# Performance work log

Measured on AMD Instinct MI355X. Metric: run time of the kernel, lower is better.

The kernel has to match this reference:

```python
import jax, jax.numpy as jnp
import numpy as np

B, T, N, F_DIM = 8, 32, 64, 6
D, H, C = 128, 4, 32          # hidden, spatial heads, head dim
L_SP, L_T, TH = 3, 3, 4       # spatial layers, temporal layers, temporal heads
THD = D // TH                 # temporal head dim
E = N * (N - 1)


def _ln(x, g, b, eps=1e-5):
    mu = x.mean(-1, keepdims=True)
    var = ((x - mu) ** 2).mean(-1, keepdims=True)
    return (x - mu) * jax.lax.rsqrt(var + eps) * g + b


def setup_inputs() -> dict:
    key = jax.random.key(0)
    ks = iter(jax.random.split(key, 64))
    r = lambda *s: jax.random.normal(next(ks), s, jnp.float32) * 0.05
    src_n, dst_n = np.nonzero(~np.eye(N, dtype=bool))
    inp = {
        'input_frames': jax.random.normal(next(ks), (B, T, N, F_DIM), jnp.float32),
        'edge_attr_seq': jax.random.uniform(next(ks), (B, T, E, 1), jnp.float32),
        'proj_W': r(F_DIM, D), 'proj_b': r(D),
        'sp_Wq': r(L_SP, D, D), 'sp_bq': r(L_SP, D),
        'sp_Wk': r(L_SP, D, D), 'sp_bk': r(L_SP, D),
        'sp_Wv': r(L_SP, D, D), 'sp_bv': r(L_SP, D),
        'sp_We': r(L_SP, 1, D), 'sp_be': r(L_SP, D),
        'sp_Ws': r(L_SP, D, D), 'sp_bs': r(L_SP, D),
        'sp_lng': jnp.ones((L_SP, D), jnp.float32), 'sp_lnb': jnp.zeros((L_SP, D), jnp.float32),
        'temporal_pos': r(1, 512, D),
        't_Wqkv': r(L_T, D, 3 * D), 't_bqkv': r(L_T, 3 * D),
        't_Wo': r(L_T, D, D), 't_bo': r(L_T, D),
        't_ln1g': jnp.ones((L_T, D), jnp.float32), 't_ln1b': jnp.zeros((L_T, D), jnp.float32),
        't_W1': r(L_T, D, 4 * D), 't_b1': r(L_T, 4 * D),
        't_W2': r(L_T, 4 * D, D), 't_b2': r(L_T, D),
        't_ln2g': jnp.ones((L_T, D), jnp.float32), 't_ln2b': jnp.zeros((L_T, D), jnp.float32),
        'head_W1': r(D, D), 'head_b1': r(D),
        'head_W2': r(D, F_DIM), 'head_b2': r(F_DIM),
        'edge_index': jnp.asarray(np.stack([src_n, dst_n]), jnp.int32),
    }
    return inp


def _forward(input_frames, edge_attr_seq, proj_W, proj_b, sp_Wq, sp_bq, sp_Wk, sp_bk,
             sp_Wv, sp_bv, sp_We, sp_be, sp_Ws, sp_bs, sp_lng, sp_lnb, temporal_pos,
             t_Wqkv, t_bqkv, t_Wo, t_bo, t_ln1g, t_ln1b, t_W1, t_b1, t_W2, t_b2,
             t_ln2g, t_ln2b, head_W1, head_b1, head_W2, head_b2, edge_index):
    BT = B * T
    Nt = BT * N                                       # total batched nodes
    offs = jnp.arange(BT, dtype=edge_index.dtype) * N
    src = (edge_index[0][None, :] + offs[:, None]).reshape(-1)   # (BT*E,)
    dst = (edge_index[1][None, :] + offs[:, None]).reshape(-1)
    ea = edge_attr_seq.reshape(BT * E, 1)
    h = input_frames.reshape(Nt, F_DIM) @ proj_W + proj_b        # (Nt, D)

    scale = 1.0 / jnp.sqrt(jnp.float32(C))
    for l in range(L_SP):
        q = (h @ sp_Wq[l] + sp_bq[l]).reshape(Nt, H, C)
        k = (h @ sp_Wk[l] + sp_bk[l]).reshape(Nt, H, C)
        v = (h @ sp_Wv[l] + sp_bv[l]).reshape(Nt, H, C)
        e = (ea @ sp_We[l] + sp_be[l]).reshape(-1, H, C)         # (Et, H, C)
        kj = k[src] + e
        alpha = (q[dst] * kj).sum(-1) * scale                    # (Et, H)
        amax = jax.ops.segment_max(alpha, dst, num_segments=Nt)
        ae = jnp.exp(alpha - amax[dst])
        asum = jax.ops.segment_sum(ae, dst, num_segments=Nt)
        w = ae / asum[dst]                                       # segment softmax
        msg = (v[src] + e) * w[..., None]
        agg = jax.ops.segment_sum(msg, dst, num_segments=Nt).reshape(Nt, D)
        out = agg + h @ sp_Ws[l] + sp_bs[l]                      # root/skip term
        h = _ln(h + out, sp_lng[l], sp_lnb[l])

    z = h.reshape(B, T, N, D).transpose(0, 2, 1, 3).reshape(B * N, T, D)
    z = z + temporal_pos[:, :T, :]

    causal = jnp.tril(jnp.ones((T, T), bool))
    tscale = 1.0 / jnp.sqrt(jnp.float32(THD))
    for l in range(L_T):
        qkv = z @ t_Wqkv[l] + t_bqkv[l]
        q, k, v = jnp.split(qkv, 3, axis=-1)
        q = q.reshape(B * N, T, TH, THD)
        k = k.reshape(B * N, T, TH, THD)
        v = v.reshape(B * N, T, TH, THD)
        s = jnp.einsum('bqhd,bkhd->bhqk', q, k) * tscale
        s = jnp.where(causal, s, -jnp.inf)
        a = jax.nn.softmax(s, axis=-1)
        o = jnp.einsum('bhqk,bkhd->bqhd', a, v).reshape(B * N, T, D)
        o = o @ t_Wo[l] + t_bo[l]
        z = _ln(z + o, t_ln1g[l], t_ln1b[l])
        f = jax.nn.gelu(z @ t_W1[l] + t_b1[l], approximate=False) @ t_W2[l] + t_b2[l]
        z = _ln(z + f, t_ln2g[l], t_ln2b[l])

    h_last = z[:, -1, :].reshape(B, N, D)
    pred = jax.nn.gelu(h_last @ head_W1 + head_b1, approximate=False) @ head_W2 + head_b2
    return pred                                                  # (B, N, F)


def reference(input_frames, edge_attr_seq, proj_W, proj_b, sp_Wq, sp_bq, sp_Wk, sp_bk,
              sp_Wv, sp_bv, sp_We, sp_be, sp_Ws, sp_bs, sp_lng, sp_lnb, temporal_pos,
              t_Wqkv, t_bqkv, t_Wo, t_bo, t_ln1g, t_ln1b, t_W1, t_b1, t_W2, t_b2,
              t_ln2g, t_ln2b, head_W1, head_b1, head_W2, head_b2, edge_index):
    return _forward(input_frames, edge_attr_seq, proj_W, proj_b, sp_Wq, sp_bq, sp_Wk,
                    sp_bk, sp_Wv, sp_bv, sp_We, sp_be, sp_Ws, sp_bs, sp_lng, sp_lnb,
                    temporal_pos, t_Wqkv, t_bqkv, t_Wo, t_bo, t_ln1g, t_ln1b, t_W1,
                    t_b1, t_W2, t_b2, t_ln2g, t_ln2b, head_W1, head_b1, head_W2,
                    head_b2, edge_index)
```

## Files before the change

kernel.cpp:

```cpp
#include <hip/hip_runtime.h>
#include <hip/hip_bf16.h>
#include <math.h>

typedef __hip_bfloat16 bf16;
typedef short short8 __attribute__((ext_vector_type(8)));
typedef float floatx4 __attribute__((ext_vector_type(4)));

#define B_    8
#define T_    32
#define N_    64
#define F_    6
#define D_    128
#define E_    4032
#define BT_   256
#define BN_   512

__device__ __forceinline__ float gelu_exact(float x) {
    return 0.5f * x * (1.0f + erff(x * 0.70710678118654752f));
}
__device__ __forceinline__ float bfbits2f(short s) {
    unsigned int u = ((unsigned int)(unsigned short)s) << 16;
    return __uint_as_float(u);
}
__device__ __forceinline__ void ld32lds(const bf16* p, float* o) {
    const short8* sp = (const short8*)p;
#pragma unroll
    for (int i = 0; i < 4; i++) {
        short8 s = sp[i];
#pragma unroll
        for (int j = 0; j < 8; j++) o[i * 8 + j] = bfbits2f(s[j]);
    }
}

struct RepackDesc { const float* W; bf16* out; int K, N, ntt, ntoff, L, start; };
struct RepackArgs { RepackDesc d[8]; int total; };

__global__ void k_repack(RepackArgs ra) {
    int gid = blockIdx.x * blockDim.x + threadIdx.x;
    if (gid >= ra.total) return;
    int fi = 0;
    while (fi < 7 && gid >= ra.d[fi + 1].start) fi++;
    RepackDesc dd = ra.d[fi];
    int r = gid - dd.start;
    int lane = r & 63; r >>= 6;
    int ntiles = dd.N >> 4;
    int nt = r % ntiles; r /= ntiles;
    int ktiles = dd.K >> 5;
    int kt = r % ktiles;
    int l = r / ktiles;
    int quad = lane >> 4, cc = lane & 15;
    const float* Wl = dd.W + (size_t)l * dd.K * dd.N;
    bf16* o = dd.out + ((((size_t)l * ktiles + kt) * dd.ntt + nt + dd.ntoff) * 64 + lane) * 8;
    int kb = kt * 32 + quad * 8;
    int n = nt * 16 + cc;
#pragma unroll
    for (int j = 0; j < 8; j++)
        o[j] = __float2bfloat16(Wl[(size_t)(kb + j) * dd.N + n]);
}

__global__ void k_packbias(const float* __restrict__ bq, const float* __restrict__ bk,
                           const float* __restrict__ bv, float* __restrict__ out) {
    int i = blockIdx.x * blockDim.x + threadIdx.x;
    if (i >= 3 * 384) return;
    int l = i / 384, c = i % 384;
    float v = (c < 128) ? bq[l * 128 + c]
            : (c < 256) ? bk[l * 128 + c - 128]
                        : bv[l * 128 + c - 256];
    out[i] = v;
}

__global__ __launch_bounds__(512, 2)
void k_spatial3(const float* __restrict__ inp, const float* __restrict__ projW,
                const float* __restrict__ projB,
                const short8* __restrict__ BpQKV, const short8* __restrict__ BpWS,
                const float* __restrict__ spb, const float* __restrict__ bs,
                const float* __restrict__ lng, const float* __restrict__ lnb,
                const float* __restrict__ ea, const float* __restrict__ Weg,
                const float* __restrict__ beg, const float* __restrict__ tpos,
                float* __restrict__ z32g) {
    __shared__ short smem[32768];
    bf16* hb = (bf16*)smem;
    bf16* qk = (bf16*)(smem + 8192);
    bf16* Ps = (bf16*)(smem + 8192);
    float* aggf = (float*)(smem + 8192);
    float* fsm = (float*)(smem + 8192);
    bf16* Vt = (bf16*)(smem + 24576);

    int bt = blockIdx.x;
    int tid = threadIdx.x;
    int lane = tid & 63, w = tid >> 6;
    int quad = lane >> 4, col = lane & 15;
    int w4 = w & 3, wh = w >> 2;
    const float scale = 0.17677669529663687f;

    for (int i = tid; i < 896; i += 512)
        fsm[i] = (i < 768) ? projW[i] : projB[i - 768];
    __syncthreads();
    float hreg[32];
    if (w < 4) {
#pragma unroll
        for (int r = 0; r < 4; r++) {
            int n = w * 16 + quad * 4 + r;
            const float* xr = inp + (size_t)(bt * 64 + n) * F_;
            float xin[6];
#pragma unroll
            for (int k2 = 0; k2 < 6; k2++) xin[k2] = xr[k2];
#pragma unroll
            for (int tt = 0; tt < 8; tt++) {
                int c = tt * 16 + col;
                float a = fsm[768 + c];
#pragma unroll
                for (int k2 = 0; k2 < 6; k2++) a = fmaf(xin[k2], fsm[k2 * 128 + c], a);
                hreg[tt * 4 + r] = a;
                hb[n * 128 + c] = __float2bfloat16(a);
            }
        }
    }
    __syncthreads();

    for (int l = 0; l < 3; l++) {
        {
            floatx4 acc[12];
#pragma unroll
            for (int tt = 0; tt < 12; tt++) acc[tt] = (floatx4){0.f, 0.f, 0.f, 0.f};
            const short8* bpl = BpQKV + (size_t)l * 6144;
            for (int kt = 0; kt < 4; kt++) {
                short8 a = *(const short8*)&hb[(w4 * 16 + col) * 128 + kt * 32 + quad * 8];
                const short8* bp = bpl + (size_t)(kt * 24 + wh * 12) * 64 + lane;
#pragma unroll
                for (int tt = 0; tt < 12; tt++)
                    acc[tt] = __builtin_amdgcn_mfma_f32_16x16x32_bf16(a, bp[tt * 64], acc[tt], 0, 0, 0);
            }
            const float* bias = spb + l * 384;
#pragma unroll
            for (int tt = 0; tt < 12; tt++) {
                int c = wh * 192 + tt * 16 + col;
                float bv = bias[c];
#pragma unroll
                for (int r = 0; r < 4; r++) {
                    int row = w4 * 16 + quad * 4 + r;
                    bf16 v = __float2bfloat16(acc[tt][r] + bv);
                    if (c < 256) qk[row * 256 + c] = v;
                    else         Vt[(c - 256) * 64 + row] = v;
                }
            }
        }
        __syncthreads();
        int h = w4, half = wh;
        int hoff = h * 32;
        const float* Wel = Weg + l * 128 + hoff;
        const float* bel = beg + l * 128 + hoff;
        float qWe;
        {
            int dst = half * 32 + (lane & 31);
            float qr[32];
            ld32lds(&qk[dst * 256 + hoff], qr);
            float s0 = 0.f;
#pragma unroll
            for (int c2 = 0; c2 < 32; c2++) s0 = fmaf(qr[c2], Wel[c2], s0);
            qWe = s0;
        }
        float s[2][4][4], ev[2][4][4];
        {
            short8 aA[2], bB[4];
#pragma unroll
            for (int mtl = 0; mtl < 2; mtl++)
                aA[mtl] = *(const short8*)&qk[((half * 2 + mtl) * 16 + col) * 256 + hoff + quad * 8];
#pragma unroll
            for (int nt = 0; nt < 4; nt++)
                bB[nt] = *(const short8*)&qk[(nt * 16 + col) * 256 + 128 + hoff + quad * 8];
#pragma unroll
            for (int mtl = 0; mtl < 2; mtl++)
#pragma unroll
                for (int nt = 0; nt < 4; nt++) {
                    floatx4 acc = (floatx4){0.f, 0.f, 0.f, 0.f};
                    acc = __builtin_amdgcn_mfma_f32_16x16x32_bf16(aA[mtl], bB[nt], acc, 0, 0, 0);
#pragma unroll
                    for (int r = 0; r < 4; r++) s[mtl][nt][r] = acc[r];
                }
        }
        const float* eag = ea + (size_t)bt * E_;
        float mx[2][4], ls[2][4], ae[2][4], inv[2][4];
#pragma unroll
        for (int mtl = 0; mtl < 2; mtl++)
#pragma unroll
            for (int r = 0; r < 4; r++) {
                int m = half * 32 + mtl * 16 + quad * 4 + r;
                float qWeR = __shfl(qWe, mtl * 16 + quad * 4 + r, 64);
                float rmax = -1e30f;
#pragma unroll
                for (int nt = 0; nt < 4; nt++) {
                    int n = nt * 16 + col;
                    bool diag = (m == n);
                    int eid = diag ? 0 : (n * 63 + m - (m > n ? 1 : 0));
                    float eav = diag ? 0.f : eag[eid];
                    ev[mtl][nt][r] = eav;
                    float al = diag ? -1e30f
                                    : scale * (s[mtl][nt][r] + eav * qWeR);
                    s[mtl][nt][r] = al;
                    rmax = fmaxf(rmax, al);
                }
#pragma unroll
                for (int mk2 = 1; mk2 <= 8; mk2 <<= 1)
                    rmax = fmaxf(rmax, __shfl_xor(rmax, mk2, 64));
                float lsum = 0.f, aesum = 0.f;
#pragma unroll
                for (int nt = 0; nt < 4; nt++) {
                    float p = __expf(s[mtl][nt][r] - rmax);
                    s[mtl][nt][r] = p;
                    lsum += p;
                    aesum = fmaf(p, ev[mtl][nt][r], aesum);
                }
#pragma unroll
                for (int mk2 = 1; mk2 <= 8; mk2 <<= 1) {
                    lsum += __shfl_xor(lsum, mk2, 64);
                    aesum += __shfl_xor(aesum, mk2, 64);
                }
                ls[mtl][r] = lsum;
                ae[mtl][r] = aesum;
                inv[mtl][r] = 1.0f / lsum;
            }
        __syncthreads();
#pragma unroll
        for (int mtl = 0; mtl < 2; mtl++)
#pragma unroll
            for (int nt = 0; nt < 4; nt++) {
                int n = nt * 16 + col;
#pragma unroll
                for (int r = 0; r < 4; r++) {
                    int m = half * 32 + mtl * 16 + quad * 4 + r;
                    Ps[h * 4096 + m * 64 + n] = __float2bfloat16(s[mtl][nt][r]);
                }
            }
        floatx4 oacc[2][2];
#pragma unroll
        for (int mtl = 0; mtl < 2; mtl++)
#pragma unroll
            for (int ntB = 0; ntB < 2; ntB++) oacc[mtl][ntB] = (floatx4){0.f, 0.f, 0.f, 0.f};
        for (int kt = 0; kt < 2; kt++) {
            short8 aP[2], bV[2];
#pragma unroll
            for (int mtl = 0; mtl < 2; mtl++)
                aP[mtl] = *(const short8*)&Ps[h * 4096 + (half * 32 + mtl * 16 + col) * 64 + kt * 32 + quad * 8];
#pragma unroll
            for (int ntB = 0; ntB < 2; ntB++)
                bV[ntB] = *(const short8*)&Vt[(hoff + ntB * 16 + col) * 64 + kt * 32 + quad * 8];
#pragma unroll
            for (int mtl = 0; mtl < 2; mtl++)
#pragma unroll
                for (int ntB = 0; ntB < 2; ntB++)
                    oacc[mtl][ntB] = __builtin_amdgcn_mfma_f32_16x16x32_bf16(aP[mtl], bV[ntB], oacc[mtl][ntB], 0, 0, 0);
        }
        __syncthreads();
#pragma unroll
        for (int mtl = 0; mtl < 2; mtl++)
#pragma unroll
            for (int ntB = 0; ntB < 2; ntB++) {
                int c = hoff + ntB * 16 + col;
                float Wc = Wel[ntB * 16 + col];
                float bc = bel[ntB * 16 + col];
#pragma unroll
                for (int r = 0; r < 4; r++) {
                    int m = half * 32 + mtl * 16 + quad * 4 + r;
                    aggf[m * 128 + c] = fmaf(fmaf(ae[mtl][r], Wc, oacc[mtl][ntB][r]),
                                             inv[mtl][r], bc);
                }
            }
        __syncthreads();
        if (w < 4) {
            floatx4 acc2[8];
#pragma unroll
            for (int tt = 0; tt < 8; tt++) acc2[tt] = (floatx4){0.f, 0.f, 0.f, 0.f};
            const short8* bpl = BpWS + (size_t)l * 2048;
            for (int kt = 0; kt < 4; kt++) {
                short8 a = *(const short8*)&hb[(w * 16 + col) * 128 + kt * 32 + quad * 8];
                const short8* bp = bpl + (size_t)(kt * 8) * 64 + lane;
#pragma unroll
                for (int tt = 0; tt < 8; tt++)
                    acc2[tt] = __builtin_amdgcn_mfma_f32_16x16x32_bf16(a, bp[tt * 64], acc2[tt], 0, 0, 0);
            }
            const float* bsl = bs + l * 128;
            float vv[32], rs[4] = {0.f, 0.f, 0.f, 0.f};
#pragma unroll
            for (int tt = 0; tt < 8; tt++) {
                int c = tt * 16 + col;
                float bv = bsl[c];
#pragma unroll
                for (int r = 0; r < 4; r++) {
                    int row = w * 16 + quad * 4 + r;
                    float v = acc2[tt][r] + bv + aggf[row * 128 + c] + hreg[tt * 4 + r];
                    vv[tt * 4 + r] = v;
                    rs[r] += v;
                }
            }
#pragma unroll
            for (int m = 1; m <= 8; m <<= 1)
#pragma unroll
                for (int r = 0; r < 4; r++) rs[r] += __shfl_xor(rs[r], m, 64);
            float mean[4], vs[4] = {0.f, 0.f, 0.f, 0.f};
#pragma unroll
            for (int r = 0; r < 4; r++) mean[r] = rs[r] * (1.0f / 128.0f);
#pragma unroll
            for (int i = 0; i < 32; i++) {
                float d = vv[i] - mean[i & 3];
                vv[i] = d;
                vs[i & 3] += d * d;
            }
#pragma unroll
            for (int m = 1; m <= 8; m <<= 1)
#pragma unroll
                for (int r = 0; r < 4; r++) vs[r] += __shfl_xor(vs[r], m, 64);
            float inv2[4];
#pragma unroll
            for (int r = 0; r < 4; r++) inv2[r] = rsqrtf(vs[r] * (1.0f / 128.0f) + 1e-5f);
            const float* gl = lng + l * 128;
            const float* bl = lnb + l * 128;
            if (l < 2) {
#pragma unroll
                for (int tt = 0; tt < 8; tt++) {
                    int c = tt * 16 + col;
                    float gc = gl[c], bc = bl[c];
#pragma unroll
                    for (int r = 0; r < 4; r++) {
                        float y = vv[tt * 4 + r] * inv2[r] * gc + bc;
                        int n = w * 16 + quad * 4 + r;
                        hreg[tt * 4 + r] = y;
                        hb[n * 128 + c] = __float2bfloat16(y);
                    }
                }
            } else {
                int b = bt >> 5, t_ = bt & 31;
#pragma unroll
                for (int tt = 0; tt < 8; tt++) {
                    int c = tt * 16 + col;
                    float gc = gl[c], bc = bl[c], pc = tpos[t_ * 128 + c];
#pragma unroll
                    for (int r = 0; r < 4; r++) {
                        float y = vv[tt * 4 + r] * inv2[r] * gc + bc;
                        int n = w * 16 + quad * 4 + r;
                        z32g[((size_t)(b * 64 + n) * 32 + t_) * 128 + c] = y + pc;
                    }
                }
            }
        }
        __syncthreads();
    }
}

__global__ __launch_bounds__(256, 2)
void k_temporal3(const float* __restrict__ z32g,
                 const short8* __restrict__ BpQKV, const short8* __restrict__ BpWO,
                 const short8* __restrict__ BpW1, const short8* __restrict__ BpW2,
                 const float* __restrict__ bqkv, const float* __restrict__ bo,
                 const float* __restrict__ ln1g, const float* __restrict__ ln1b,
                 const float* __restrict__ b1, const float* __restrict__ b2,
                 const float* __restrict__ ln2g, const float* __restrict__ ln2b,
                 float* __restrict__ zlast) {
    __shared__ short smem[27392];
    bf16* zb  = (bf16*)smem;
    bf16* qk  = (bf16*)(smem + 4352);
    bf16* Ps  = (bf16*)(smem + 12800);
    bf16* Vt  = (bf16*)(smem + 17920);
    bf16* o16 = (bf16*)(smem + 23040);
    bf16* f1  = (bf16*)(smem + 4352);

    int bn = blockIdx.x;
    int tid = threadIdx.x;
    int lane = tid & 63, w = tid >> 6;
    int quad = lane >> 4, col = lane & 15;
    int rsel = w & 1, csel = w >> 1;
    const float scale = 0.17677669529663687f;

    for (int i = tid; i < 4096; i += 256) {
        float v = z32g[(size_t)bn * 4096 + i];
        zb[(i >> 7) * 136 + (i & 127)] = __float2bfloat16(v);
    }
    float zreg[32];
    if (w < 2) {
#pragma unroll
        for (int tt = 0; tt < 8; tt++)
#pragma unroll
            for (int r = 0; r < 4; r++)
                zreg[tt * 4 + r] = z32g[(size_t)bn * 4096 +
                                        (w * 16 + quad * 4 + r) * 128 + tt * 16 + col];
    }
    __syncthreads();

    for (int l = 0; l < 3; l++) {
        {
            floatx4 acc[12];
#pragma unroll
            for (int tt = 0; tt < 12; tt++) acc[tt] = (floatx4){0.f, 0.f, 0.f, 0.f};
            const short8* bpl = BpQKV + (size_t)l * 6144;
            for (int kt = 0; kt < 4; kt++) {
                short8 a = *(const short8*)&zb[(rsel * 16 + col) * 136 + kt * 32 + quad * 8];
                const short8* bp = bpl + (size_t)(kt * 24 + csel * 12) * 64 + lane;
#pragma unroll
                for (int tt = 0; tt < 12; tt++)
                    acc[tt] = __builtin_amdgcn_mfma_f32_16x16x32_bf16(a, bp[tt * 64], acc[tt], 0, 0, 0);
            }
            const float* bias = bqkv + l * 384;
#pragma unroll
            for (int tt = 0; tt < 12; tt++) {
                int c = csel * 192 + tt * 16 + col;
                float bv = bias[c];
#pragma unroll
                for (int r = 0; r < 4; r++) {
                    int row = rsel * 16 + quad * 4 + r;
                    bf16 v = __float2bfloat16(acc[tt][r] + bv);
                    if (c < 256) qk[row * 264 + c] = v;
                    else         Vt[(c - 256) * 40 + row] = v;
                }
            }
        }
        __syncthreads();
        {
            int h = w, hoff = h * 32;
            float s[2][2][4];
            short8 aA[2], bB[2];
#pragma unroll
            for (int mt = 0; mt < 2; mt++)
                aA[mt] = *(const short8*)&qk[(mt * 16 + col) * 264 + hoff + quad * 8];
#pragma unroll
            for (int nt = 0; nt < 2; nt++)
                bB[nt] = *(const short8*)&qk[(nt * 16 + col) * 264 + 128 + hoff + quad * 8];
#pragma unroll
            for (int mt = 0; mt < 2; mt++)
#pragma unroll
                for (int nt = 0; nt < 2; nt++) {
                    floatx4 acc = (floatx4){0.f, 0.f, 0.f, 0.f};
                    acc = __builtin_amdgcn_mfma_f32_16x16x32_bf16(aA[mt], bB[nt], acc, 0, 0, 0);
#pragma unroll
                    for (int r = 0; r < 4; r++) s[mt][nt][r] = acc[r];
                }
            float inv[2][4];
#pragma unroll
            for (int mt = 0; mt < 2; mt++)
#pragma unroll
                for (int r = 0; r < 4; r++) {
                    int m = mt * 16 + quad * 4 + r;
                    float rmax = -1e30f;
#pragma unroll
                    for (int nt = 0; nt < 2; nt++) {
                        int n = nt * 16 + col;
                        float al = (n > m) ? -1e30f : s[mt][nt][r] * scale;
                        s[mt][nt][r] = al;
                        rmax = fmaxf(rmax, al);
                    }
#pragma unroll
                    for (int mk2 = 1; mk2 <= 8; mk2 <<= 1)
                        rmax = fmaxf(rmax, __shfl_xor(rmax, mk2, 64));
                    float lsum = 0.f;
#pragma unroll
                    for (int nt = 0; nt < 2; nt++) {
                        float p = __expf(s[mt][nt][r] - rmax);
                        s[mt][nt][r] = p;
                        lsum += p;
                    }
#pragma unroll
                    for (int mk2 = 1; mk2 <= 8; mk2 <<= 1)
                        lsum += __shfl_xor(lsum, mk2, 64);
                    inv[mt][r] = 1.0f / lsum;
                }
#pragma unroll
            for (int mt = 0; mt < 2; mt++)
#pragma unroll
                for (int nt = 0; nt < 2; nt++) {
                    int n = nt * 16 + col;
#pragma unroll
                    for (int r = 0; r < 4; r++)
                        Ps[h * 1280 + (mt * 16 + quad * 4 + r) * 40 + n] =
                            __float2bfloat16(s[mt][nt][r]);
                }
            floatx4 oacc[2][2];
#pragma unroll
            for (int mt = 0; mt < 2; mt++)
#pragma unroll
                for (int nt = 0; nt < 2; nt++) oacc[mt][nt] = (floatx4){0.f, 0.f, 0.f, 0.f};
            short8 aP[2], bV[2];
#pragma unroll
            for (int mt = 0; mt < 2; mt++)
                aP[mt] = *(const short8*)&Ps[h * 1280 + (mt * 16 + col) * 40 + quad * 8];
#pragma unroll
            for (int nt = 0; nt < 2; nt++)
                bV[nt] = *(const short8*)&Vt[(hoff + nt * 16 + col) * 40 + quad * 8];
#pragma unroll
            for (int mt = 0; mt < 2; mt++)
#pragma unroll
                for (int nt = 0; nt < 2; nt++)
                    oacc[mt][nt] = __builtin_amdgcn_mfma_f32_16x16x32_bf16(aP[mt], bV[nt], oacc[mt][nt], 0, 0, 0);
#pragma unroll
            for (int mt = 0; mt < 2; mt++)
#pragma unroll
                for (int nt = 0; nt < 2; nt++) {
                    int c = hoff + nt * 16 + col;
#pragma unroll
                    for (int r = 0; r < 4; r++)
                        o16[(mt * 16 + quad * 4 + r) * 136 + c] =
                            __float2bfloat16(oacc[mt][nt][r] * inv[mt][r]);
                }
        }
        __syncthreads();
        if (w < 2) {
            floatx4 acc2[8];
#pragma unroll
            for (int tt = 0; tt < 8; tt++) acc2[tt] = (floatx4){0.f, 0.f, 0.f, 0.f};
            const short8* bpl = BpWO + (size_t)l * 2048;
            for (int kt = 0; kt < 4; kt++) {
                short8 a = *(const short8*)&o16[(w * 16 + col) * 136 + kt * 32 + quad * 8];
                const short8* bp = bpl + (size_t)(kt * 8) * 64 + lane;
#pragma unroll
                for (int tt = 0; tt < 8; tt++)
                    acc2[tt] = __builtin_amdgcn_mfma_f32_16x16x32_bf16(a, bp[tt * 64], acc2[tt], 0, 0, 0);
            }
            const float* bol = bo + l * 128;
            float vv[32], rs[4] = {0.f, 0.f, 0.f, 0.f};
#pragma unroll
            for (int tt = 0; tt < 8; tt++) {
                int c = tt * 16 + col;
                float bv = bol[c];
#pragma unroll
                for (int r = 0; r < 4; r++) {
                    float v = acc2[tt][r] + bv + zreg[tt * 4 + r];
                    vv[tt * 4 + r] = v;
                    rs[r] += v;
                }
            }
#pragma unroll
            for (int m = 1; m <= 8; m <<= 1)
#pragma unroll
                for (int r = 0; r < 4; r++) rs[r] += __shfl_xor(rs[r], m, 64);
            float mean[4], vs[4] = {0.f, 0.f, 0.f, 0.f};
#pragma unroll
            for (int r = 0; r < 4; r++) mean[r] = rs[r] * (1.0f / 128.0f);
#pragma unroll
            for (int i = 0; i < 32; i++) {
                float d = vv[i] - mean[i & 3];
                vv[i] = d;
                vs[i & 3] += d * d;
            }
#pragma unroll
            for (int m = 1; m <= 8; m <<= 1)
#pragma unroll
                for (int r = 0; r < 4; r++) vs[r] += __shfl_xor(vs[r], m, 64);
            float inv2[4];
#pragma unroll
            for (int r = 0; r < 4; r++) inv2[r] = rsqrtf(vs[r] * (1.0f / 128.0f) + 1e-5f);
            const float* gl = ln1g + l * 128;
            const float* bl = ln1b + l * 128;
#pragma unroll
            for (int tt = 0; tt < 8; tt++) {
                int c = tt * 16 + col;
                float gc = gl[c], bc = bl[c];
#pragma unroll
                for (int r = 0; r < 4; r++) {
                    float y = vv[tt * 4 + r] * inv2[r] * gc + bc;
                    int row = w * 16 + quad * 4 + r;
                    zreg[tt * 4 + r] = y;
                    zb[row * 136 + c] = __float2bfloat16(y);
                }
            }
        }
        __syncthreads();
        {
            floatx4 acc3[16];
#pragma unroll
            for (int tt = 0; tt < 16; tt++) acc3[tt] = (floatx4){0.f, 0.f, 0.f, 0.f};
            const short8* bpl = BpW1 + (size_t)l * 8192;
            for (int kt = 0; kt < 4; kt++) {
                short8 a = *(const short8*)&zb[(rsel * 16 + col) * 136 + kt * 32 + quad * 8];
                const short8* bp = bpl + (size_t)(kt * 32 + csel * 16) * 64 + lane;
#pragma unroll
                for (int tt = 0; tt < 16; tt++)
                    acc3[tt] = __builtin_amdgcn_mfma_f32_16x16x32_bf16(a, bp[tt * 64], acc3[tt], 0, 0, 0);
            }
            const float* b1l = b1 + l * 512;
#pragma unroll
            for (int tt = 0; tt < 16; tt++) {
                int c = csel * 256 + tt * 16 + col;
                float bv = b1l[c];
#pragma unroll
                for (int r = 0; r < 4; r++) {
                    float v = gelu_exact(acc3[tt][r] + bv);
                    f1[(rsel * 16 + quad * 4 + r) * 520 + c] = __float2bfloat16(v);
                }
            }
        }
        __syncthreads();
        if (w < 2) {
            floatx4 acc4[8];
#pragma unroll
            for (int tt = 0; tt < 8; tt++) acc4[tt] = (floatx4){0.f, 0.f, 0.f, 0.f};
            const short8* bpl = BpW2 + (size_t)l * 8192;
            for (int kt = 0; kt < 16; kt++) {
                short8 a = *(const short8*)&f1[(w * 16 + col) * 520 + kt * 32 + quad * 8];
                const short8* bp = bpl + (size_t)(kt * 8) * 64 + lane;
#pragma unroll
                for (int tt = 0; tt < 8; tt++)
                    acc4[tt] = __builtin_amdgcn_mfma_f32_16x16x32_bf16(a, bp[tt * 64], acc4[tt], 0, 0, 0);
            }
            const float* b2l = b2 + l * 128;
            float vv[32], rs[4] = {0.f, 0.f, 0.f, 0.f};
#pragma unroll
            for (int tt = 0; tt < 8; tt++) {
                int c = tt * 16 + col;
                float bv = b2l[c];
#pragma unroll
                for (int r = 0; r < 4; r++) {
                    float v = acc4[tt][r] + bv + zreg[tt * 4 + r];
                    vv[tt * 4 + r] = v;
                    rs[r] += v;
                }
            }
#pragma unroll
            for (int m = 1; m <= 8; m <<= 1)
#pragma unroll
                for (int r = 0; r < 4; r++) rs[r] += __shfl_xor(rs[r], m, 64);
            float mean[4], vs[4] = {0.f, 0.f, 0.f, 0.f};
#pragma unroll
            for (int r = 0; r < 4; r++) mean[r] = rs[r] * (1.0f / 128.0f);
#pragma unroll
            for (int i = 0; i < 32; i++) {
                float d = vv[i] - mean[i & 3];
                vv[i] = d;
                vs[i & 3] += d * d;
            }
#pragma unroll
            for (int m = 1; m <= 8; m <<= 1)
#pragma unroll
                for (int r = 0; r < 4; r++) vs[r] += __shfl_xor(vs[r], m, 64);
            float inv2[4];
#pragma unroll
            for (int r = 0; r < 4; r++) inv2[r] = rsqrtf(vs[r] * (1.0f / 128.0f) + 1e-5f);
            const float* gl = ln2g + l * 128;
            const float* bl = ln2b + l * 128;
#pragma unroll
            for (int tt = 0; tt < 8; tt++) {
                int c = tt * 16 + col;
                float gc = gl[c], bc = bl[c];
#pragma unroll
                for (int r = 0; r < 4; r++) {
                    float y = vv[tt * 4 + r] * inv2[r] * gc + bc;
                    int row = w * 16 + quad * 4 + r;
                    zreg[tt * 4 + r] = y;
                    if (l < 2) zb[row * 136 + c] = __float2bfloat16(y);
                    else if (row == 31) zlast[(size_t)bn * 128 + c] = y;
                }
            }
        }
        __syncthreads();
    }
}

__global__ __launch_bounds__(128)
void k_head(const float* __restrict__ zlast, const float* __restrict__ W1,
            const float* __restrict__ b1, const float* __restrict__ W2,
            const float* __restrict__ b2, float* __restrict__ out) {
    int bn = blockIdx.x;
    int d = threadIdx.x;
    __shared__ float zl[128], h1[128];
    zl[d] = zlast[(size_t)bn * 128 + d];
    __syncthreads();
    float acc = b1[d];
    for (int k = 0; k < 128; k++) acc = fmaf(zl[k], W1[k * 128 + d], acc);
    h1[d] = gelu_exact(acc);
    __syncthreads();
    if (d < F_) {
        float o = b2[d];
        for (int k = 0; k < 128; k++) o = fmaf(h1[k], W2[k * F_ + d], o);
        out[bn * F_ + d] = o;
    }
}

extern "C" void kernel_launch(void* const* d_in, const int* in_sizes, int n_in,
                              void* d_out, int out_size, void* d_ws, size_t ws_size,
                              hipStream_t stream) {
    const float* input_frames = (const float*)d_in[0];
    const float* edge_attr    = (const float*)d_in[1];
    const float* proj_W  = (const float*)d_in[2];
    const float* proj_b  = (const float*)d_in[3];
    const float* sp_Wq   = (const float*)d_in[4];
    const float* sp_bq   = (const float*)d_in[5];
    const float* sp_Wk   = (const float*)d_in[6];
    const float* sp_bk   = (const float*)d_in[7];
    const float* sp_Wv   = (const float*)d_in[8];
    const float* sp_bv   = (const float*)d_in[9];
    const float* sp_We   = (const float*)d_in[10];
    const float* sp_be   = (const float*)d_in[11];
    const float* sp_Ws   = (const float*)d_in[12];
    const float* sp_bs   = (const float*)d_in[13];
    const float* sp_lng  = (const float*)d_in[14];
    const float* sp_lnb  = (const float*)d_in[15];
    const float* tpos    = (const float*)d_in[16];
    const float* t_Wqkv  = (const float*)d_in[17];
    const float* t_bqkv  = (const float*)d_in[18];
    const float* t_Wo    = (const float*)d_in[19];
    const float* t_bo    = (const float*)d_in[20];
    const float* t_ln1g  = (const float*)d_in[21];
    const float* t_ln1b  = (const float*)d_in[22];
    const float* t_W1    = (const float*)d_in[23];
    const float* t_b1    = (const float*)d_in[24];
    const float* t_W2    = (const float*)d_in[25];
    const float* t_b2    = (const float*)d_in[26];
    const float* t_ln2g  = (const float*)d_in[27];
    const float* t_ln2b  = (const float*)d_in[28];
    const float* head_W1 = (const float*)d_in[29];
    const float* head_b1 = (const float*)d_in[30];
    const float* head_W2 = (const float*)d_in[31];
    const float* head_b2 = (const float*)d_in[32];

    float* f     = (float*)d_ws;
    float* z32g  = f;
    float* zlast = f + (1u << 21);
    float* spb   = f + (1u << 21) + 65536;
    bf16* BpBase = (bf16*)(f + (1u << 21) + 65536 + 2048);
    bf16* BpSPQKV = BpBase;
    bf16* BpWS    = BpSPQKV + 147456;
    bf16* BpTQKV  = BpWS + 49152;
    bf16* BpWO    = BpTQKV + 147456;
    bf16* BpW1    = BpWO + 49152;
    bf16* BpW2    = BpW1 + 196608;

    RepackArgs ra;
    int s = 0;
    auto mk = [&](int i, const float* W, bf16* out, int K, int N, int ntt, int ntoff, int L) {
        ra.d[i] = {W, out, K, N, ntt, ntoff, L, s};
        s += L * (K >> 5) * (N >> 4) * 64;
    };
    mk(0, sp_Wq, BpSPQKV, 128, 128, 24, 0, 3);
    mk(1, sp_Wk, BpSPQKV, 128, 128, 24, 8, 3);
    mk(2, sp_Wv, BpSPQKV, 128, 128, 24, 16, 3);
    mk(3, sp_Ws, BpWS, 128, 128, 8, 0, 3);
    mk(4, t_Wqkv, BpTQKV, 128, 384, 24, 0, 3);
    mk(5, t_Wo, BpWO, 128, 128, 8, 0, 3);
    mk(6, t_W1, BpW1, 128, 512, 32, 0, 3);
    mk(7, t_W2, BpW2, 512, 128, 8, 0, 3);
    ra.total = s;
    k_repack<<<(s + 255) / 256, 256, 0, stream>>>(ra);
    k_packbias<<<(3 * 384 + 255) / 256, 256, 0, stream>>>(sp_bq, sp_bk, sp_bv, spb);

    k_spatial3<<<BT_, 512, 0, stream>>>(
        input_frames, proj_W, proj_b,
        (const short8*)BpSPQKV, (const short8*)BpWS,
        spb, sp_bs, sp_lng, sp_lnb, edge_attr, sp_We, sp_be, tpos, z32g);

    k_temporal3<<<BN_, 256, 0, stream>>>(
        z32g, (const short8*)BpTQKV, (const short8*)BpWO,
        (const short8*)BpW1, (const short8*)BpW2,
        t_bqkv, t_bo, t_ln1g, t_ln1b, t_b1, t_b2, t_ln2g, t_ln2b, zlast);

    k_head<<<BN_, 128, 0, stream>>>(zlast, head_W1, head_b1, head_W2, head_b2,
                                    (float*)d_out);
}
```

Measured before the change: 312.9 us.

## Pad LDS layouts, stage edge attrs, split-bf16 P·V, MFMA head kernel

Several changes at once. The spatial kernel pads its LDS rows to reduce bank conflicts and stages each block's edge attributes into LDS. It gives P its own buffer so one barrier can be removed, at the cost of dropping occupancy to one block per CU. Both attention kernels store P as hi/lo bf16 pairs and run two MFMAs per tile for accuracy, which doubles that work. The head kernel is rewritten to use MFMA over 64 rows per block with bf16 zlast input, replacing 512 tiny blocks of scalar FMA loops.

```diff
diff --git a/kernel.cpp b/kernel.cpp
--- a/kernel.cpp
+++ b/kernel.cpp
@@ -33,13 +33,13 @@
 }
 
 struct RepackDesc { const float* W; bf16* out; int K, N, ntt, ntoff, L, start; };
-struct RepackArgs { RepackDesc d[8]; int total; };
+struct RepackArgs { RepackDesc d[9]; int total; };
 
 __global__ void k_repack(RepackArgs ra) {
     int gid = blockIdx.x * blockDim.x + threadIdx.x;
     if (gid >= ra.total) return;
     int fi = 0;
-    while (fi < 7 && gid >= ra.d[fi + 1].start) fi++;
+    while (fi < 8 && gid >= ra.d[fi + 1].start) fi++;
     RepackDesc dd = ra.d[fi];
     int r = gid - dd.start;
     int lane = r & 63; r >>= 6;
@@ -69,7 +69,7 @@
     out[i] = v;
 }
 
-__global__ __launch_bounds__(512, 2)
+__global__ __launch_bounds__(512, 1)
 void k_spatial3(const float* __restrict__ inp, const float* __restrict__ projW,
                 const float* __restrict__ projB,
                 const short8* __restrict__ BpQKV, const short8* __restrict__ BpWS,
@@ -78,13 +78,14 @@
                 const float* __restrict__ ea, const float* __restrict__ Weg,
                 const float* __restrict__ beg, const float* __restrict__ tpos,
                 float* __restrict__ z32g) {
-    __shared__ short smem[32768];
+    __shared__ short smem[61312];
     bf16* hb = (bf16*)smem;
-    bf16* qk = (bf16*)(smem + 8192);
-    bf16* Ps = (bf16*)(smem + 8192);
-    float* aggf = (float*)(smem + 8192);
-    float* fsm = (float*)(smem + 8192);
-    bf16* Vt = (bf16*)(smem + 24576);
+    bf16* qk = (bf16*)(smem + 8704);
+    float* aggf = (float*)(smem + 8704);
+    float* fsm = (float*)(smem + 8704);
+    bf16* Vt = (bf16*)(smem + 25600);
+    bf16* Ps = (bf16*)(smem + 34816);
+    float* EAs = (float*)(smem + 53248);
 
     int bt = blockIdx.x;
     int tid = threadIdx.x;
@@ -95,6 +96,10 @@
 
     for (int i = tid; i < 896; i += 512)
         fsm[i] = (i < 768) ? projW[i] : projB[i - 768];
+    {
+        const float* eag = ea + (size_t)bt * E_;
+        for (int i = tid; i < E_; i += 512) EAs[i] = eag[i];
+    }
     __syncthreads();
     float hreg[32];
     if (w < 4) {
@@ -112,7 +117,7 @@
 #pragma unroll
                 for (int k2 = 0; k2 < 6; k2++) a = fmaf(xin[k2], fsm[k2 * 128 + c], a);
                 hreg[tt * 4 + r] = a;
-                hb[n * 128 + c] = __float2bfloat16(a);
+                hb[n * 136 + c] = __float2bfloat16(a);
             }
         }
     }
@@ -125,7 +130,7 @@
             for (int tt = 0; tt < 12; tt++) acc[tt] = (floatx4){0.f, 0.f, 0.f, 0.f};
             const short8* bpl = BpQKV + (size_t)l * 6144;
             for (int kt = 0; kt < 4; kt++) {
-                short8 a = *(const short8*)&hb[(w4 * 16 + col) * 128 + kt * 32 + quad * 8];
+                short8 a = *(const short8*)&hb[(w4 * 16 + col) * 136 + kt * 32 + quad * 8];
                 const short8* bp = bpl + (size_t)(kt * 24 + wh * 12) * 64 + lane;
 #pragma unroll
                 for (int tt = 0; tt < 12; tt++)
@@ -140,8 +145,8 @@
                 for (int r = 0; r < 4; r++) {
                     int row = w4 * 16 + quad * 4 + r;
                     bf16 v = __float2bfloat16(acc[tt][r] + bv);
-                    if (c < 256) qk[row * 256 + c] = v;
-                    else         Vt[(c - 256) * 64 + row] = v;
+                    if (c < 256) qk[row * 264 + c] = v;
+                    else         Vt[(c - 256) * 72 + row] = v;
                 }
             }
         }
@@ -154,21 +159,26 @@
         {
             int dst = half * 32 + (lane & 31);
             float qr[32];
-            ld32lds(&qk[dst * 256 + hoff], qr);
-            float s0 = 0.f;
-#pragma unroll
-            for (int c2 = 0; c2 < 32; c2++) s0 = fmaf(qr[c2], Wel[c2], s0);
-            qWe = s0;
+            ld32lds(&qk[dst * 264 + hoff], qr);
+            float s0 = 0.f, s1 = 0.f, s2 = 0.f, s3 = 0.f;
+#pragma unroll
+            for (int c2 = 0; c2 < 32; c2 += 4) {
+                s0 = fmaf(qr[c2], Wel[c2], s0);
+                s1 = fmaf(qr[c2 + 1], Wel[c2 + 1], s1);
+                s2 = fmaf(qr[c2 + 2], Wel[c2 + 2], s2);
+                s3 = fmaf(qr[c2 + 3], Wel[c2 + 3], s3);
+            }
+            qWe = (s0 + s1) + (s2 + s3);
         }
         float s[2][4][4], ev[2][4][4];
         {
             short8 aA[2], bB[4];
 #pragma unroll
             for (int mtl = 0; mtl < 2; mtl++)
-                aA[mtl] = *(const short8*)&qk[((half * 2 + mtl) * 16 + col) * 256 + hoff + quad * 8];
+                aA[mtl] = *(const short8*)&qk[((half * 2 + mtl) * 16 + col) * 264 + hoff + quad * 8];
 #pragma unroll
             for (int nt = 0; nt < 4; nt++)
-                bB[nt] = *(const short8*)&qk[(nt * 16 + col) * 256 + 128 + hoff + quad * 8];
+                bB[nt] = *(const short8*)&qk[(nt * 16 + col) * 264 + 128 + hoff + quad * 8];
 #pragma unroll
             for (int mtl = 0; mtl < 2; mtl++)
 #pragma unroll
@@ -179,8 +189,8 @@
                     for (int r = 0; r < 4; r++) s[mtl][nt][r] = acc[r];
                 }
         }
-        const float* eag = ea + (size_t)bt * E_;
-        float mx[2][4], ls[2][4], ae[2][4], inv[2][4];
+        __syncthreads();
+        float ls[2][4], ae[2][4], inv[2][4];
 #pragma unroll
         for (int mtl = 0; mtl < 2; mtl++)
 #pragma unroll
@@ -193,7 +203,7 @@
                     int n = nt * 16 + col;
                     bool diag = (m == n);
                     int eid = diag ? 0 : (n * 63 + m - (m > n ? 1 : 0));
-                    float eav = diag ? 0.f : eag[eid];
+                    float eav = diag ? 0.f : EAs[eid];
                     ev[mtl][nt][r] = eav;
                     float al = diag ? -1e30f
                                     : scale * (s[mtl][nt][r] + eav * qWeR);
@@ -220,38 +230,47 @@
                 ae[mtl][r] = aesum;
                 inv[mtl][r] = 1.0f / lsum;
             }
-        __syncthreads();
+        bf16* PsH = Ps + h * 4608;
+        floatx4 oacc[2][2];
 #pragma unroll
         for (int mtl = 0; mtl < 2; mtl++)
 #pragma unroll
-            for (int nt = 0; nt < 4; nt++) {
-                int n = nt * 16 + col;
-#pragma unroll
-                for (int r = 0; r < 4; r++) {
-                    int m = half * 32 + mtl * 16 + quad * 4 + r;
-                    Ps[h * 4096 + m * 64 + n] = __float2bfloat16(s[mtl][nt][r]);
-                }
-            }
-        floatx4 oacc[2][2];
-#pragma unroll
-        for (int mtl = 0; mtl < 2; mtl++)
-#pragma unroll
             for (int ntB = 0; ntB < 2; ntB++) oacc[mtl][ntB] = (floatx4){0.f, 0.f, 0.f, 0.f};
-        for (int kt = 0; kt < 2; kt++) {
-            short8 aP[2], bV[2];
+#pragma unroll
+        for (int p = 0; p < 2; p++) {
 #pragma unroll
             for (int mtl = 0; mtl < 2; mtl++)
-                aP[mtl] = *(const short8*)&Ps[h * 4096 + (half * 32 + mtl * 16 + col) * 64 + kt * 32 + quad * 8];
+#pragma unroll
+                for (int q2 = 0; q2 < 2; q2++) {
+                    int nl = q2 * 16 + col;
+                    int base0 = (half * 32 + mtl * 16 + quad * 4) * 72 + ((nl >> 3) * 2) * 8 + (nl & 7);
+#pragma unroll
+                    for (int r = 0; r < 4; r++) {
+                        float p_ = s[mtl][2 * p + q2][r];
+                        bf16 hi = __float2bfloat16(p_);
+                        bf16 lo = __float2bfloat16(p_ - bfbits2f(*(short*)&hi));
+                        PsH[base0 + r * 72] = hi;
+                        PsH[base0 + r * 72 + 8] = lo;
+                    }
+                }
+            short8 aPh[2], aPl[2], bV[2];
+#pragma unroll
+            for (int mtl = 0; mtl < 2; mtl++) {
+                int rb = (half * 32 + mtl * 16 + col) * 72 + quad * 16;
+                aPh[mtl] = *(const short8*)&PsH[rb];
+                aPl[mtl] = *(const short8*)&PsH[rb + 8];
+            }
 #pragma unroll
             for (int ntB = 0; ntB < 2; ntB++)
-                bV[ntB] = *(const short8*)&Vt[(hoff + ntB * 16 + col) * 64 + kt * 32 + quad * 8];
+                bV[ntB] = *(const short8*)&Vt[(hoff + ntB * 16 + col) * 72 + p * 32 + quad * 8];
 #pragma unroll
             for (int mtl = 0; mtl < 2; mtl++)
 #pragma unroll
-                for (int ntB = 0; ntB < 2; ntB++)
-                    oacc[mtl][ntB] = __builtin_amdgcn_mfma_f32_16x16x32_bf16(aP[mtl], bV[ntB], oacc[mtl][ntB], 0, 0, 0);
-        }
-        __syncthreads();
+                for (int ntB = 0; ntB < 2; ntB++) {
+                    oacc[mtl][ntB] = __builtin_amdgcn_mfma_f32_16x16x32_bf16(aPh[mtl], bV[ntB], oacc[mtl][ntB], 0, 0, 0);
+                    oacc[mtl][ntB] = __builtin_amdgcn_mfma_f32_16x16x32_bf16(aPl[mtl], bV[ntB], oacc[mtl][ntB], 0, 0, 0);
+                }
+        }
 #pragma unroll
         for (int mtl = 0; mtl < 2; mtl++)
 #pragma unroll
@@ -273,7 +292,7 @@
             for (int tt = 0; tt < 8; tt++) acc2[tt] = (floatx4){0.f, 0.f, 0.f, 0.f};
             const short8* bpl = BpWS + (size_t)l * 2048;
             for (int kt = 0; kt < 4; kt++) {
-                short8 a = *(const short8*)&hb[(w * 16 + col) * 128 + kt * 32 + quad * 8];
+                short8 a = *(const short8*)&hb[(w * 16 + col) * 136 + kt * 32 + quad * 8];
                 const short8* bp = bpl + (size_t)(kt * 8) * 64 + lane;
 #pragma unroll
                 for (int tt = 0; tt < 8; tt++)
@@ -325,7 +344,7 @@
                         float y = vv[tt * 4 + r] * inv2[r] * gc + bc;
                         int n = w * 16 + quad * 4 + r;
                         hreg[tt * 4 + r] = y;
-                        hb[n * 128 + c] = __float2bfloat16(y);
+                        hb[n * 136 + c] = __float2bfloat16(y);
                     }
                 }
             } else {
@@ -355,13 +374,13 @@
                  const float* __restrict__ ln1g, const float* __restrict__ ln1b,
                  const float* __restrict__ b1, const float* __restrict__ b2,
                  const float* __restrict__ ln2g, const float* __restrict__ ln2b,
-                 float* __restrict__ zlast) {
-    __shared__ short smem[27392];
+                 bf16* __restrict__ zlastb) {
+    __shared__ short smem[31488];
     bf16* zb  = (bf16*)smem;
     bf16* qk  = (bf16*)(smem + 4352);
     bf16* Ps  = (bf16*)(smem + 12800);
-    bf16* Vt  = (bf16*)(smem + 17920);
-    bf16* o16 = (bf16*)(smem + 23040);
+    bf16* Vt  = (bf16*)(smem + 22016);
+    bf16* o16 = (bf16*)(smem + 27136);
     bf16* f1  = (bf16*)(smem + 4352);
 
     int bn = blockIdx.x;
@@ -416,6 +435,7 @@
         __syncthreads();
         {
             int h = w, hoff = h * 32;
+            bf16* PsH = Ps + h * 2304;
             float s[2][2][4];
             short8 aA[2], bB[2];
 #pragma unroll
@@ -467,28 +487,38 @@
 #pragma unroll
                 for (int nt = 0; nt < 2; nt++) {
                     int n = nt * 16 + col;
-#pragma unroll
-                    for (int r = 0; r < 4; r++)
-                        Ps[h * 1280 + (mt * 16 + quad * 4 + r) * 40 + n] =
-                            __float2bfloat16(s[mt][nt][r]);
+                    int base0 = (mt * 16 + quad * 4) * 72 + ((n >> 3) * 2) * 8 + (n & 7);
+#pragma unroll
+                    for (int r = 0; r < 4; r++) {
+                        float p_ = s[mt][nt][r];
+                        bf16 hi = __float2bfloat16(p_);
+                        bf16 lo = __float2bfloat16(p_ - bfbits2f(*(short*)&hi));
+                        PsH[base0 + r * 72] = hi;
+                        PsH[base0 + r * 72 + 8] = lo;
+                    }
                 }
             floatx4 oacc[2][2];
 #pragma unroll
             for (int mt = 0; mt < 2; mt++)
 #pragma unroll
                 for (int nt = 0; nt < 2; nt++) oacc[mt][nt] = (floatx4){0.f, 0.f, 0.f, 0.f};
-            short8 aP[2], bV[2];
-#pragma unroll
-            for (int mt = 0; mt < 2; mt++)
-                aP[mt] = *(const short8*)&Ps[h * 1280 + (mt * 16 + col) * 40 + quad * 8];
+            short8 aPh[2], aPl[2], bV[2];
+#pragma unroll
+            for (int mt = 0; mt < 2; mt++) {
+                int rb = (mt * 16 + col) * 72 + quad * 16;
+                aPh[mt] = *(const short8*)&PsH[rb];
+                aPl[mt] = *(const short8*)&PsH[rb + 8];
+            }
 #pragma unroll
             for (int nt = 0; nt < 2; nt++)
                 bV[nt] = *(const short8*)&Vt[(hoff + nt * 16 + col) * 40 + quad * 8];
 #pragma unroll
             for (int mt = 0; mt < 2; mt++)
 #pragma unroll
-                for (int nt = 0; nt < 2; nt++)
-                    oacc[mt][nt] = __builtin_amdgcn_mfma_f32_16x16x32_bf16(aP[mt], bV[nt], oacc[mt][nt], 0, 0, 0);
+                for (int nt = 0; nt < 2; nt++) {
+                    oacc[mt][nt] = __builtin_amdgcn_mfma_f32_16x16x32_bf16(aPh[mt], bV[nt], oacc[mt][nt], 0, 0, 0);
+                    oacc[mt][nt] = __builtin_amdgcn_mfma_f32_16x16x32_bf16(aPl[mt], bV[nt], oacc[mt][nt], 0, 0, 0);
+                }
 #pragma unroll
             for (int mt = 0; mt < 2; mt++)
 #pragma unroll
@@ -644,7 +674,7 @@
                     int row = w * 16 + quad * 4 + r;
                     zreg[tt * 4 + r] = y;
                     if (l < 2) zb[row * 136 + c] = __float2bfloat16(y);
-                    else if (row == 31) zlast[(size_t)bn * 128 + c] = y;
+                    else if (row == 31) zlastb[(size_t)bn * 128 + c] = __float2bfloat16(y);
                 }
             }
         }
@@ -652,23 +682,51 @@
     }
 }
 
-__global__ __launch_bounds__(128)
-void k_head(const float* __restrict__ zlast, const float* __restrict__ W1,
+__global__ __launch_bounds__(256)
+void k_head(const bf16* __restrict__ zlastb, const short8* __restrict__ BpHW1,
             const float* __restrict__ b1, const float* __restrict__ W2,
             const float* __restrict__ b2, float* __restrict__ out) {
-    int bn = blockIdx.x;
-    int d = threadIdx.x;
-    __shared__ float zl[128], h1[128];
-    zl[d] = zlast[(size_t)bn * 128 + d];
+    __shared__ bf16 h1[64 * 136];
+    int blk = blockIdx.x;
+    int tid = threadIdx.x;
+    int lane = tid & 63, w = tid >> 6;
+    int quad = lane >> 4, col = lane & 15;
+    {
+        floatx4 acc[8];
+#pragma unroll
+        for (int tt = 0; tt < 8; tt++) acc[tt] = (floatx4){0.f, 0.f, 0.f, 0.f};
+        const short8* Ap = (const short8*)(zlastb + (size_t)(blk * 64 + w * 16 + col) * 128) + quad;
+        for (int kt = 0; kt < 4; kt++) {
+            short8 a = Ap[kt * 4];
+            const short8* bp = BpHW1 + (size_t)(kt * 8) * 64 + lane;
+#pragma unroll
+            for (int tt = 0; tt < 8; tt++)
+                acc[tt] = __builtin_amdgcn_mfma_f32_16x16x32_bf16(a, bp[tt * 64], acc[tt], 0, 0, 0);
+        }
+#pragma unroll
+        for (int tt = 0; tt < 8; tt++) {
+            int c = tt * 16 + col;
+            float bv = b1[c];
+#pragma unroll
+            for (int r = 0; r < 4; r++)
+                h1[(w * 16 + quad * 4 + r) * 136 + c] = __float2bfloat16(gelu_exact(acc[tt][r] + bv));
+        }
+    }
     __syncthreads();
-    float acc = b1[d];
-    for (int k = 0; k < 128; k++) acc = fmaf(zl[k], W1[k * 128 + d], acc);
-    h1[d] = gelu_exact(acc);
-    __syncthreads();
-    if (d < F_) {
-        float o = b2[d];
-        for (int k = 0; k < 128; k++) o = fmaf(h1[k], W2[k * F_ + d], o);
-        out[bn * F_ + d] = o;
+    for (int idx = tid; idx < 512; idx += 256) {
+        int row = idx >> 3, c = idx & 7;
+        if (c < 6) {
+            float a0 = 0.f, a1 = 0.f, a2 = 0.f, a3 = 0.f;
+            const bf16* hr = &h1[row * 136];
+#pragma unroll 8
+            for (int k = 0; k < 128; k += 4) {
+                a0 = fmaf(bfbits2f(*(const short*)&hr[k]),     W2[k * 6 + c], a0);
+                a1 = fmaf(bfbits2f(*(const short*)&hr[k + 1]), W2[(k + 1) * 6 + c], a1);
+                a2 = fmaf(bfbits2f(*(const short*)&hr[k + 2]), W2[(k + 2) * 6 + c], a2);
+                a3 = fmaf(bfbits2f(*(const short*)&hr[k + 3]), W2[(k + 3) * 6 + c], a3);
+            }
+            out[(size_t)(blk * 64 + row) * 6 + c] = (a0 + a1) + (a2 + a3) + b2[c];
+        }
     }
 }
 
@@ -711,7 +769,7 @@
 
     float* f     = (float*)d_ws;
     float* z32g  = f;
-    float* zlast = f + (1u << 21);
+    bf16*  zlastb = (bf16*)(f + (1u << 21));
     float* spb   = f + (1u << 21) + 65536;
     bf16* BpBase = (bf16*)(f + (1u << 21) + 65536 + 2048);
     bf16* BpSPQKV = BpBase;
@@ -720,6 +778,7 @@
     bf16* BpWO    = BpTQKV + 147456;
     bf16* BpW1    = BpWO + 49152;
     bf16* BpW2    = BpW1 + 196608;
+    bf16* BpHW1   = BpW2 + 196608;
 
     RepackArgs ra;
     int s = 0;
@@ -735,6 +794,7 @@
     mk(5, t_Wo, BpWO, 128, 128, 8, 0, 3);
     mk(6, t_W1, BpW1, 128, 512, 32, 0, 3);
     mk(7, t_W2, BpW2, 512, 128, 8, 0, 3);
+    mk(8, head_W1, BpHW1, 128, 128, 8, 0, 1);
     ra.total = s;
     k_repack<<<(s + 255) / 256, 256, 0, stream>>>(ra);
     k_packbias<<<(3 * 384 + 255) / 256, 256, 0, stream>>>(sp_bq, sp_bk, sp_bv, spb);
@@ -747,8 +807,8 @@
     k_temporal3<<<BN_, 256, 0, stream>>>(
         z32g, (const short8*)BpTQKV, (const short8*)BpWO,
         (const short8*)BpW1, (const short8*)BpW2,
-        t_bqkv, t_bo, t_ln1g, t_ln1b, t_b1, t_b2, t_ln2g, t_ln2b, zlast);
-
-    k_head<<<BN_, 128, 0, stream>>>(zlast, head_W1, head_b1, head_W2, head_b2,
-                                    (float*)d_out);
+        t_bqkv, t_bo, t_ln1g, t_ln1b, t_b1, t_b2, t_ln2g, t_ln2b, zlastb);
+
+    k_head<<<8, 256, 0, stream>>>(zlastb, (const short8*)BpHW1, head_b1,
+                                  head_W2, head_b2, (float*)d_out);
 }
```

After: 289.5 us. 1.08x faster.
